# Performance work log

Hardware: AMD Instinct MI355X
Metric: run time of the kernel (lower is better)

Reference implementation:

```python
import jax, jax.numpy as jnp
import numpy as np

B, S, D, H = 2, 2048, 768, 12
DK = D // H

def setup_inputs() -> dict:
    key = jax.random.key(0)
    ks = jax.random.split(key, 8)
    query = jax.random.normal(ks[0], (B, S, D), dtype=jnp.float32)
    key_t = jax.random.normal(ks[1], (B, S, D), dtype=jnp.float32)
    value = jax.random.normal(ks[2], (B, S, D), dtype=jnp.float32)
    # causal (look-ahead) mask: True above the diagonal -> masked
    mask = jnp.triu(jnp.ones((S, S), dtype=bool), k=1)[None, None]  # (1,1,S,S)
    scale = 1.0 / np.sqrt(D)
    w_q = jax.random.normal(ks[3], (D, D), dtype=jnp.float32) * scale
    w_k = jax.random.normal(ks[4], (D, D), dtype=jnp.float32) * scale
    w_v = jax.random.normal(ks[5], (D, D), dtype=jnp.float32) * scale
    w_o = jax.random.normal(ks[6], (D, D), dtype=jnp.float32) * scale
    return {"query": query, "key": key_t, "value": value, "mask": mask,
            "w_q": w_q, "w_k": w_k, "w_v": w_v, "w_o": w_o}

def reference(query, key, value, mask, w_q, w_k, w_v, w_o):
    b = query.shape[0]
    # nn.Linear(bias=False): y = x @ W.T
    q = (query @ w_q.T).reshape(b, -1, H, DK).transpose(0, 2, 1, 3)  # (B,H,Sq,dk)
    k = (key @ w_k.T).reshape(b, -1, H, DK).transpose(0, 2, 1, 3)    # (B,H,Sk,dk)
    v = (value @ w_v.T).reshape(b, -1, H, DK).transpose(0, 2, 1, 3)  # (B,H,Sk,dk)
    scores = jnp.einsum('bhqd,bhkd->bhqk', q, k) / jnp.sqrt(jnp.float32(DK))
    scores = jnp.where(mask, jnp.float32(-1e9), scores)
    attn_weights = jax.nn.softmax(scores, axis=-1)  # (B,H,Sq,Sk); dropout=0 (eval)
    context = jnp.einsum('bhqk,bhkd->bhqd', attn_weights, v)
    context = context.transpose(0, 2, 1, 3).reshape(b, -1, D)
    output = context @ w_o.T
    return output, attn_weights
```

## Files before the change

### kernel.cpp

```cpp
#include <hip/hip_runtime.h>

#define BATCH 2
#define S_LEN 2048
#define NH 12
#define DMODEL 768

#define N8_BSD (BATCH * S_LEN * DMODEL / 8)
#define N8_DD (DMODEL * DMODEL / 8)

typedef __attribute__((ext_vector_type(8))) short bf16x8;
typedef __attribute__((ext_vector_type(4))) float f32x4;
typedef __attribute__((ext_vector_type(4))) unsigned short us4;

__device__ __forceinline__ unsigned short f2bf(float f) {
  union { float f; unsigned int u; } v; v.f = f;
  unsigned int r = v.u + 0x7fffu + ((v.u >> 16) & 1u);
  return (unsigned short)(r >> 16);
}

__global__ void cvt3_kernel(const float* __restrict__ s0,
                            const float* __restrict__ s1,
                            const float* __restrict__ s2,
                            unsigned short* __restrict__ dst) {
  int i = blockIdx.x * blockDim.x + threadIdx.x;
  int j = i / N8_BSD;
  int k = i - j * N8_BSD;
  const float* s = (j == 0) ? s0 : (j == 1) ? s1 : s2;
  const float4* sp = (const float4*)s;
  float4 a = sp[k * 2], b = sp[k * 2 + 1];
  us4 o0 = { f2bf(a.x), f2bf(a.y), f2bf(a.z), f2bf(a.w) };
  us4 o1 = { f2bf(b.x), f2bf(b.y), f2bf(b.z), f2bf(b.w) };
  us4* d = (us4*)dst;
  d[i * 2] = o0;
  d[i * 2 + 1] = o1;
}

__global__ void cvt4_kernel(const float* __restrict__ s0,
                            const float* __restrict__ s1,
                            const float* __restrict__ s2,
                            const float* __restrict__ s3,
                            unsigned short* __restrict__ dst) {
  int i = blockIdx.x * blockDim.x + threadIdx.x;
  int j = i / N8_DD;
  int k = i - j * N8_DD;
  const float* s = (j == 0) ? s0 : (j == 1) ? s1 : (j == 2) ? s2 : s3;
  const float4* sp = (const float4*)s;
  float4 a = sp[k * 2], b = sp[k * 2 + 1];
  us4 o0 = { f2bf(a.x), f2bf(a.y), f2bf(a.z), f2bf(a.w) };
  us4 o1 = { f2bf(b.x), f2bf(b.y), f2bf(b.z), f2bf(b.w) };
  us4* d = (us4*)dst;
  d[i * 2] = o0;
  d[i * 2 + 1] = o1;
}

__global__ void ctx_reduce(const float* __restrict__ c0,
                           const float* __restrict__ c1,
                           unsigned short* __restrict__ o) {
  int i = blockIdx.x * blockDim.x + threadIdx.x;
  int s = (i / 192) & (S_LEN - 1);
  float4 a = ((const float4*)c0)[i];
  float4 r = a;
  if (s >= 1024) {
    float4 b = ((const float4*)c1)[i];
    r.x += b.x; r.y += b.y; r.z += b.z; r.w += b.w;
  }
  us4 u = { f2bf(r.x), f2bf(r.y), f2bf(r.z), f2bf(r.w) };
  ((us4*)o)[i] = u;
}

#define GLD_LDS16(g, l)                                                    \
  __builtin_amdgcn_global_load_lds(                                        \
      (const __attribute__((address_space(1))) unsigned int*)(g),          \
      (__attribute__((address_space(3))) unsigned int*)(l), 16, 0, 0)

__global__ __launch_bounds__(256, 2)
void gemm_qkv(const unsigned short* __restrict__ Aq,
              const unsigned short* __restrict__ Ak,
              const unsigned short* __restrict__ Av,
              const unsigned short* __restrict__ W3,
              unsigned short* __restrict__ Qs,
              unsigned short* __restrict__ Ks,
              unsigned short* __restrict__ VT) {
  __shared__ unsigned short As[128 * 64];
  __shared__ unsigned short Bs[128 * 64];
  const int m0 = blockIdx.x * 128;
  const int n0g = blockIdx.y * 128;
  const int nblk = n0g / 768;
  const int n0 = n0g - nblk * 768;
  const unsigned short* A = (nblk == 0) ? Aq : (nblk == 1) ? Ak : Av;
  const unsigned short* Bw = W3 + (size_t)n0g * DMODEL;
  const int tid = threadIdx.x, w = tid >> 6, l = tid & 63;
  const int lg = l >> 4, ll = l & 15;
  const int wm = w >> 1, wn = w & 1;
  const int lr = l >> 3, lc = (l & 7) * 8;

  f32x4 acc[4][4];
#pragma unroll
  for (int i = 0; i < 4; ++i)
#pragma unroll
    for (int j = 0; j < 4; ++j) acc[i][j] = (f32x4){0.f, 0.f, 0.f, 0.f};

  for (int k0 = 0; k0 < DMODEL; k0 += 64) {
#pragma unroll
    for (int i = 0; i < 4; ++i) {
      GLD_LDS16(A + (size_t)(m0 + w * 32 + i * 8 + lr) * DMODEL + k0 + lc,
                &As[(w * 32 + i * 8) * 64]);
      GLD_LDS16(Bw + (size_t)(w * 32 + i * 8 + lr) * DMODEL + k0 + lc,
                &Bs[(w * 32 + i * 8) * 64]);
    }
    __syncthreads();
#pragma unroll
    for (int t = 0; t < 2; ++t) {
      bf16x8 af[4], bf[4];
#pragma unroll
      for (int mi = 0; mi < 4; ++mi)
        af[mi] = *(const bf16x8*)&As[(wm * 64 + mi * 16 + ll) * 64 + t * 32 + lg * 8];
#pragma unroll
      for (int ni = 0; ni < 4; ++ni)
        bf[ni] = *(const bf16x8*)&Bs[(wn * 64 + ni * 16 + ll) * 64 + t * 32 + lg * 8];
#pragma unroll
      for (int mi = 0; mi < 4; ++mi)
#pragma unroll
        for (int ni = 0; ni < 4; ++ni)
          acc[mi][ni] = __builtin_amdgcn_mfma_f32_16x16x32_bf16(
              af[mi], bf[ni], acc[mi][ni], 0, 0, 0);
    }
    __syncthreads();
  }

  if (nblk < 2) {
    unsigned short* o = nblk ? Ks : Qs;
    const float sc = nblk ? 1.f : 0.125f;
#pragma unroll
    for (int mi = 0; mi < 4; ++mi)
#pragma unroll
      for (int ni = 0; ni < 4; ++ni) {
        const int col = n0 + wn * 64 + ni * 16 + ll;
        const int rowb = m0 + wm * 64 + mi * 16 + lg * 4;
#pragma unroll
        for (int r = 0; r < 4; ++r)
          o[(size_t)(rowb + r) * 768 + col] = f2bf(acc[mi][ni][r] * sc);
      }
  } else {
#pragma unroll
    for (int mi = 0; mi < 4; ++mi)
#pragma unroll
      for (int ni = 0; ni < 4; ++ni) {
        const int col = n0 + wn * 64 + ni * 16 + ll;
        const int row = m0 + wm * 64 + mi * 16 + lg * 4;
        const int bb = row >> 11, sidx = row & (S_LEN - 1);
        const size_t base =
            ((size_t)(bb * NH + (col >> 6)) * 64 + (col & 63)) * S_LEN + sidx;
        us4 pk = { f2bf(acc[mi][ni][0]), f2bf(acc[mi][ni][1]),
                   f2bf(acc[mi][ni][2]), f2bf(acc[mi][ni][3]) };
        *(us4*)&VT[base] = pk;
      }
  }
}

__global__ __launch_bounds__(256, 2)
void gemm_proj(const unsigned short* __restrict__ A,
               const unsigned short* __restrict__ Bw,
               float* __restrict__ o) {
  __shared__ unsigned short As[128 * 64];
  __shared__ unsigned short Bs[128 * 64];
  const int m0 = blockIdx.x * 128, n0 = blockIdx.y * 128;
  const int tid = threadIdx.x, w = tid >> 6, l = tid & 63;
  const int lg = l >> 4, ll = l & 15;
  const int wm = w >> 1, wn = w & 1;
  const int lr = l >> 3, lc = (l & 7) * 8;

  f32x4 acc[4][4];
#pragma unroll
  for (int i = 0; i < 4; ++i)
#pragma unroll
    for (int j = 0; j < 4; ++j) acc[i][j] = (f32x4){0.f, 0.f, 0.f, 0.f};

  for (int k0 = 0; k0 < DMODEL; k0 += 64) {
#pragma unroll
    for (int i = 0; i < 4; ++i) {
      GLD_LDS16(A + (size_t)(m0 + w * 32 + i * 8 + lr) * DMODEL + k0 + lc,
                &As[(w * 32 + i * 8) * 64]);
      GLD_LDS16(Bw + (size_t)(n0 + w * 32 + i * 8 + lr) * DMODEL + k0 + lc,
                &Bs[(w * 32 + i * 8) * 64]);
    }
    __syncthreads();
#pragma unroll
    for (int t = 0; t < 2; ++t) {
      bf16x8 af[4], bf[4];
#pragma unroll
      for (int mi = 0; mi < 4; ++mi)
        af[mi] = *(const bf16x8*)&As[(wm * 64 + mi * 16 + ll) * 64 + t * 32 + lg * 8];
#pragma unroll
      for (int ni = 0; ni < 4; ++ni)
        bf[ni] = *(const bf16x8*)&Bs[(wn * 64 + ni * 16 + ll) * 64 + t * 32 + lg * 8];
#pragma unroll
      for (int mi = 0; mi < 4; ++mi)
#pragma unroll
        for (int ni = 0; ni < 4; ++ni)
          acc[mi][ni] = __builtin_amdgcn_mfma_f32_16x16x32_bf16(
              af[mi], bf[ni], acc[mi][ni], 0, 0, 0);
    }
    __syncthreads();
  }

#pragma unroll
  for (int mi = 0; mi < 4; ++mi)
#pragma unroll
    for (int ni = 0; ni < 4; ++ni) {
      const int col = n0 + wn * 64 + ni * 16 + ll;
      const int rowb = m0 + wm * 64 + mi * 16 + lg * 4;
#pragma unroll
      for (int r = 0; r < 4; ++r)
        o[(size_t)(rowb + r) * DMODEL + col] = acc[mi][ni][r];
    }
}

#define STAGE_TILE(srcTile, srcStride, ldsT)                                  \
  {                                                                           \
    _Pragma("unroll") for (int j_ = 0; j_ < 2; ++j_) {                        \
      int slot_ = (j_ * 4 + w) * 64 + l;                                      \
      int row_ = slot_ >> 3, c16_ = slot_ & 7;                                \
      GLD_LDS16((srcTile) + (size_t)row_ * (srcStride) +                      \
                    ((c16_ ^ (row_ & 7)) << 3),                               \
                (ldsT) + (j_ * 4 + w) * 512);                                 \
    }                                                                         \
  }

__global__ __launch_bounds__(256, 3)
void attn_ml(const unsigned short* __restrict__ Qp,
             const unsigned short* __restrict__ Kp,
             float2* __restrict__ mlbuf) {
  const int idx = blockIdx.x;
  const int qt = 31 - idx / (NH * BATCH);
  const int hb = idx % (NH * BATCH);
  const int h = hb >> 1, b = hb & 1;
  const int tid = threadIdx.x, w = tid >> 6, l = tid & 63;
  const int lg = l >> 4, ll = l & 15;
  __shared__ unsigned short Kt[2][64 * 64];

  const unsigned short* kbp = Kp + (size_t)b * S_LEN * DMODEL + h * 64;
  const int q0 = qt * 64 + w * 16;
  const int nkt = qt + 1;

  bf16x8 qf[2];
  {
    const unsigned short* qb =
        Qp + (size_t)(b * S_LEN + q0 + ll) * DMODEL + h * 64 + lg * 8;
    qf[0] = *(const bf16x8*)qb;
    qf[1] = *(const bf16x8*)(qb + 32);
  }
  int rowg[4];
#pragma unroll
  for (int r = 0; r < 4; ++r) rowg[r] = q0 + lg * 4 + r;

  float m[4], lsum[4];
#pragma unroll
  for (int r = 0; r < 4; ++r) { m[r] = -1e30f; lsum[r] = 0.f; }

  STAGE_TILE(kbp + (size_t)0 * 64 * DMODEL, DMODEL, &Kt[0][0]);
  __syncthreads();

  for (int kt = 0; kt < nkt; ++kt) {
    const int cur = kt & 1;
    if (kt + 1 < nkt)
      STAGE_TILE(kbp + (size_t)(kt + 1) * 64 * DMODEL, DMODEL, &Kt[cur ^ 1][0]);
    bf16x8 kf[8];
#pragma unroll
    for (int t = 0; t < 2; ++t)
#pragma unroll
      for (int nb = 0; nb < 4; ++nb) {
        const int row = nb * 16 + ll;
        kf[t * 4 + nb] = *(const bf16x8*)&Kt[cur][row * 64 +
            (((t * 4 + lg) ^ (row & 7)) << 3)];
      }
    f32x4 sv[4];
#pragma unroll
    for (int nb = 0; nb < 4; ++nb) sv[nb] = (f32x4){0.f, 0.f, 0.f, 0.f};
#pragma unroll
    for (int t = 0; t < 2; ++t)
#pragma unroll
      for (int nb = 0; nb < 4; ++nb)
        sv[nb] = __builtin_amdgcn_mfma_f32_16x16x32_bf16(qf[t], kf[t * 4 + nb],
                                                         sv[nb], 0, 0, 0);
    if (kt == nkt - 1) {
#pragma unroll
      for (int nb = 0; nb < 4; ++nb) {
        const int col = kt * 64 + nb * 16 + ll;
#pragma unroll
        for (int r = 0; r < 4; ++r)
          if (col > rowg[r]) sv[nb][r] = -1e30f;
      }
    }
#pragma unroll
    for (int r = 0; r < 4; ++r) {
      float tm = fmaxf(fmaxf(sv[0][r], sv[1][r]), fmaxf(sv[2][r], sv[3][r]));
      float mn = fmaxf(m[r], tm);
      float te = __expf(sv[0][r] - mn) + __expf(sv[1][r] - mn) +
                 __expf(sv[2][r] - mn) + __expf(sv[3][r] - mn);
      lsum[r] = lsum[r] * __expf(m[r] - mn) + te;
      m[r] = mn;
    }
    __syncthreads();
  }

#pragma unroll
  for (int off = 1; off < 16; off <<= 1)
#pragma unroll
    for (int r = 0; r < 4; ++r) {
      float om = __shfl_xor(m[r], off, 64);
      float ol = __shfl_xor(lsum[r], off, 64);
      float mn = fmaxf(m[r], om);
      lsum[r] = lsum[r] * __expf(m[r] - mn) + ol * __expf(om - mn);
      m[r] = mn;
    }

  if (ll == 0) {
    float2* mlb = mlbuf + (size_t)(b * NH + h) * S_LEN;
#pragma unroll
    for (int r = 0; r < 4; ++r)
      mlb[rowg[r]] = make_float2(m[r], 1.f / lsum[r]);
  }
}

__global__ __launch_bounds__(256, 2)
void attn_p2(const unsigned short* __restrict__ Qp,
             const unsigned short* __restrict__ Kp,
             const unsigned short* __restrict__ VTp,
             const float2* __restrict__ mlbuf,
             float* __restrict__ attnw,
             float* __restrict__ ctx0,
             float* __restrict__ ctx1) {
  const int idx = blockIdx.x;
  const int hb = idx >> 6;
  const int slot = idx & 63;
  const int h = hb >> 1, b = hb & 1;
  int qt, ck;
  if (slot <= 16)      { ck = 0; qt = 15 + slot; }
  else if (slot == 17) { ck = 1; qt = 31; }
  else if (slot < 48)  { int u = slot - 18; int k = 15 - (u >> 1);
                         if (u & 1) { ck = 1; qt = k + 15; } else { ck = 0; qt = k - 1; } }
  else                 { ck = 1; qt = slot - 48; }

  const int ktlo = ck * 16;
  const int kthi = (qt < ktlo + 15) ? qt : (ktlo + 15);
  const bool hasval = (ktlo <= qt);

  const int tid = threadIdx.x, w = tid >> 6, l = tid & 63;
  const int lg = l >> 4, ll = l & 15;
  __shared__ float pf32[4][64 * 64];
  float* pfw = &pf32[w][0];

  const unsigned short* kbp = Kp + (size_t)b * S_LEN * DMODEL + h * 64;
  const unsigned short* vbp = VTp + ((size_t)(b * NH + h)) * 64 * S_LEN;
  float* pbase = attnw + ((size_t)(b * NH + h)) * S_LEN * S_LEN;
  const int q0g = qt * 64;

  if (hasval) {
    bf16x8 qf[4][2];
#pragma unroll
    for (int rb = 0; rb < 4; ++rb) {
      const unsigned short* qb =
          Qp + (size_t)(b * S_LEN + q0g + rb * 16 + ll) * DMODEL + h * 64 + lg * 8;
      qf[rb][0] = *(const bf16x8*)qb;
      qf[rb][1] = *(const bf16x8*)(qb + 32);
    }
    float m16[4][4], li16[4][4];
    {
      const float2* mlb = mlbuf + (size_t)(b * NH + h) * S_LEN;
#pragma unroll
      for (int rb = 0; rb < 4; ++rb)
#pragma unroll
        for (int r = 0; r < 4; ++r) {
          float2 t = mlb[q0g + rb * 16 + lg * 4 + r];
          m16[rb][r] = t.x;
          li16[rb][r] = t.y;
        }
    }

    f32x4 cacc[4][4];
#pragma unroll
    for (int rb = 0; rb < 4; ++rb)
#pragma unroll
      for (int vb = 0; vb < 4; ++vb) cacc[rb][vb] = (f32x4){0.f, 0.f, 0.f, 0.f};

    for (int kt = ktlo + w; kt <= kthi; kt += 4) {
#pragma unroll
      for (int hh = 0; hh < 2; ++hh) {
        bf16x8 kf[2][2];
#pragma unroll
        for (int t = 0; t < 2; ++t)
#pragma unroll
          for (int nbl = 0; nbl < 2; ++nbl) {
            const int nb = hh * 2 + nbl;
            kf[t][nbl] = *(const bf16x8*)(kbp +
                (size_t)(kt * 64 + nb * 16 + ll) * DMODEL + t * 32 + lg * 8);
          }
        f32x4 sv[4][2];
#pragma unroll
        for (int rb = 0; rb < 4; ++rb)
#pragma unroll
          for (int nbl = 0; nbl < 2; ++nbl) sv[rb][nbl] = (f32x4){0.f, 0.f, 0.f, 0.f};
#pragma unroll
        for (int t = 0; t < 2; ++t)
#pragma unroll
          for (int rb = 0; rb < 4; ++rb)
#pragma unroll
            for (int nbl = 0; nbl < 2; ++nbl)
              sv[rb][nbl] = __builtin_amdgcn_mfma_f32_16x16x32_bf16(
                  qf[rb][t], kf[t][nbl], sv[rb][nbl], 0, 0, 0);
#pragma unroll
        for (int nbl = 0; nbl < 2; ++nbl) {
          const int nb = hh * 2 + nbl;
          const int col = kt * 64 + nb * 16 + ll;
#pragma unroll
          for (int rb = 0; rb < 4; ++rb)
#pragma unroll
            for (int r = 0; r < 4; ++r) {
              const int row = q0g + rb * 16 + lg * 4 + r;
              float p = (col <= row)
                            ? __expf(sv[rb][nbl][r] - m16[rb][r]) * li16[rb][r]
                            : 0.f;
              pfw[(rb * 16 + lg * 4 + r) * 64 +
                  ((nb * 16 + ll) ^ ((lg & 1) << 4))] = p;
            }
        }
      }
#pragma unroll
      for (int t = 0; t < 2; ++t) {
        bf16x8 pfr[4];
#pragma unroll
        for (int rb = 0; rb < 4; ++rb) {
          const int row = rb * 16 + ll;
          const int c0 = (t * 32 + lg * 8) ^ (((ll >> 2) & 1) << 4);
          f32x4 lo = *(const f32x4*)&pfw[row * 64 + c0];
          f32x4 hi = *(const f32x4*)&pfw[row * 64 + c0 + 4];
          union { us4 hh2[2]; bf16x8 v; } u;
          u.hh2[0] = (us4){ f2bf(lo[0]), f2bf(lo[1]), f2bf(lo[2]), f2bf(lo[3]) };
          u.hh2[1] = (us4){ f2bf(hi[0]), f2bf(hi[1]), f2bf(hi[2]), f2bf(hi[3]) };
          pfr[rb] = u.v;
        }
        bf16x8 vf[4];
#pragma unroll
        for (int vb = 0; vb < 4; ++vb)
          vf[vb] = *(const bf16x8*)(vbp +
              (size_t)(vb * 16 + ll) * S_LEN + kt * 64 + t * 32 + lg * 8);
#pragma unroll
        for (int rb = 0; rb < 4; ++rb)
#pragma unroll
          for (int vb = 0; vb < 4; ++vb)
            cacc[rb][vb] = __builtin_amdgcn_mfma_f32_16x16x32_bf16(
                pfr[rb], vf[vb], cacc[rb][vb], 0, 0, 0);
      }
#pragma unroll
      for (int ps = 0; ps < 16; ++ps) {
        const int row = ps * 4 + lg;
        const int cb = (ll * 4) ^ ((ps & 1) << 4);
        f32x4 pv = *(const f32x4*)&pfw[row * 64 + cb];
        __builtin_nontemporal_store(
            pv, (f32x4*)&pbase[(size_t)(q0g + row) * S_LEN + kt * 64 + ll * 4]);
      }
    }

#pragma unroll
    for (int rb = 0; rb < 4; ++rb)
#pragma unroll
      for (int vb = 0; vb < 4; ++vb)
#pragma unroll
        for (int r = 0; r < 4; ++r)
          pfw[(rb * 16 + lg * 4 + r) * 64 +
              ((vb * 16 + ll) ^ ((lg & 1) << 4))] = cacc[rb][vb][r];
    __syncthreads();
    float* co = ck ? ctx1 : ctx0;
#pragma unroll
    for (int ps2 = 0; ps2 < 4; ++ps2) {
      const int row = w * 16 + ps2 * 4 + lg;
      const int cb = (ll * 4) ^ ((ps2 & 1) << 4);
      f32x4 s0 = *(const f32x4*)&pf32[0][row * 64 + cb];
      f32x4 s1 = *(const f32x4*)&pf32[1][row * 64 + cb];
      f32x4 s2 = *(const f32x4*)&pf32[2][row * 64 + cb];
      f32x4 s3 = *(const f32x4*)&pf32[3][row * 64 + cb];
      f32x4 sm = (s0 + s1) + (s2 + s3);
      *(f32x4*)&co[(size_t)(b * S_LEN + q0g + row) * DMODEL + h * 64 + ll * 4] = sm;
    }
  }

  const int q0w = qt * 64 + w * 16;
  const int zs = ((qt + 1) * 64 > ktlo * 64) ? (qt + 1) * 64 : ktlo * 64;
  const int ze = (ktlo + 16) * 64;
  if (zs < ze) {
    f32x4 z = (f32x4){0.f, 0.f, 0.f, 0.f};
    for (int rr = 0; rr < 16; ++rr) {
      float* dst = pbase + (size_t)(q0w + rr) * S_LEN;
      for (int c = zs + l * 4; c < ze; c += 256)
        __builtin_nontemporal_store(z, (f32x4*)(dst + c));
    }
  }
}

extern "C" void kernel_launch(void* const* d_in, const int* in_sizes, int n_in,
                              void* d_out, int out_size, void* d_ws, size_t ws_size,
                              hipStream_t stream) {
  const float* q_in = (const float*)d_in[0];
  const float* k_in = (const float*)d_in[1];
  const float* v_in = (const float*)d_in[2];
  const float* wq = (const float*)d_in[4];
  const float* wk = (const float*)d_in[5];
  const float* wv = (const float*)d_in[6];
  const float* wo = (const float*)d_in[7];

  const int BSD = BATCH * S_LEN * DMODEL;
  const int DD = DMODEL * DMODEL;
  const int M = BATCH * S_LEN;

  char* ws = (char*)d_ws;
  unsigned short* qbf = (unsigned short*)ws;  ws += (size_t)BSD * 2;
  unsigned short* kbf = (unsigned short*)ws;  ws += (size_t)BSD * 2;
  unsigned short* vbf = (unsigned short*)ws;  ws += (size_t)BSD * 2;
  unsigned short* wqb = (unsigned short*)ws;  ws += (size_t)DD * 2;
  unsigned short* wkb = (unsigned short*)ws;  ws += (size_t)DD * 2;
  unsigned short* wvb = (unsigned short*)ws;  ws += (size_t)DD * 2;
  unsigned short* wob = (unsigned short*)ws;  ws += (size_t)DD * 2;
  unsigned short* Qs  = (unsigned short*)ws;  ws += (size_t)BSD * 2;
  unsigned short* Ks  = (unsigned short*)ws;  ws += (size_t)BSD * 2;
  unsigned short* VT  = (unsigned short*)ws;  ws += (size_t)BSD * 2;
  unsigned short* ctx = (unsigned short*)ws;  ws += (size_t)BSD * 2;
  float* ctx0 = (float*)ws;                   ws += (size_t)BSD * 4;
  float* ctx1 = (float*)ws;                   ws += (size_t)BSD * 4;
  float2* mlbuf = (float2*)ws;                ws += (size_t)M * NH * sizeof(float2);
  (void)wkb; (void)wvb;

  float* out_proj = (float*)d_out;
  float* attnw = (float*)d_out + BSD;

  cvt3_kernel<<<3 * N8_BSD / 256, 256, 0, stream>>>(q_in, k_in, v_in, qbf);
  cvt4_kernel<<<4 * N8_DD / 256, 256, 0, stream>>>(wq, wk, wv, wo, wqb);

  gemm_qkv<<<dim3(M / 128, 2304 / 128), 256, 0, stream>>>(qbf, kbf, vbf, wqb,
                                                          Qs, Ks, VT);

  attn_ml<<<32 * NH * BATCH, 256, 0, stream>>>(Qs, Ks, mlbuf);
  attn_p2<<<64 * NH * BATCH, 256, 0, stream>>>(Qs, Ks, VT, mlbuf, attnw,
                                               ctx0, ctx1);
  ctx_reduce<<<BSD / 4 / 256, 256, 0, stream>>>(ctx0, ctx1, ctx);

  gemm_proj<<<dim3(M / 128, DMODEL / 128), 256, 0, stream>>>(ctx, wob, out_proj);
}
```

Baseline: 189.7 us.

## Split attention p2 blocks into 32-row query halves and reorder ml grid

The attn_p2 kernel now processes 32 query rows per block instead of 64. This doubles the grid, halves shared memory per block and cuts register pressure, so launch bounds can request 3 blocks per CU. Each K tile is still loaded once per 32-row block, so K/V global loads per output row double, traded for better occupancy and load balance. The attn_ml block index mapping is also changed so that consecutive blocks share a head and batch, which is meant to improve K locality in cache.

```diff
diff --git a/kernel.cpp b/kernel.cpp
--- a/kernel.cpp
+++ b/kernel.cpp
@@ -232,8 +232,8 @@
              const unsigned short* __restrict__ Kp,
              float2* __restrict__ mlbuf) {
   const int idx = blockIdx.x;
-  const int qt = 31 - idx / (NH * BATCH);
-  const int hb = idx % (NH * BATCH);
+  const int hb = idx >> 5;
+  const int qt = 31 - (idx & 31);
   const int h = hb >> 1, b = hb & 1;
   const int tid = threadIdx.x, w = tid >> 6, l = tid & 63;
   const int lg = l >> 4, ll = l & 15;
@@ -323,7 +323,7 @@
   }
 }
 
-__global__ __launch_bounds__(256, 2)
+__global__ __launch_bounds__(256, 3)
 void attn_p2(const unsigned short* __restrict__ Qp,
              const unsigned short* __restrict__ Kp,
              const unsigned short* __restrict__ VTp,
@@ -332,8 +332,10 @@
              float* __restrict__ ctx0,
              float* __restrict__ ctx1) {
   const int idx = blockIdx.x;
-  const int hb = idx >> 6;
-  const int slot = idx & 63;
+  const int hb = idx >> 7;
+  const int sl = idx & 127;
+  const int slot = sl >> 1;
+  const int qh = sl & 1;
   const int h = hb >> 1, b = hb & 1;
   int qt, ck;
   if (slot <= 16)      { ck = 0; qt = 15 + slot; }
@@ -348,28 +350,28 @@
 
   const int tid = threadIdx.x, w = tid >> 6, l = tid & 63;
   const int lg = l >> 4, ll = l & 15;
-  __shared__ float pf32[4][64 * 64];
+  __shared__ float pf32[4][32 * 64];
   float* pfw = &pf32[w][0];
 
   const unsigned short* kbp = Kp + (size_t)b * S_LEN * DMODEL + h * 64;
   const unsigned short* vbp = VTp + ((size_t)(b * NH + h)) * 64 * S_LEN;
   float* pbase = attnw + ((size_t)(b * NH + h)) * S_LEN * S_LEN;
-  const int q0g = qt * 64;
+  const int q0g = qt * 64 + qh * 32;
 
   if (hasval) {
-    bf16x8 qf[4][2];
-#pragma unroll
-    for (int rb = 0; rb < 4; ++rb) {
+    bf16x8 qf[2][2];
+#pragma unroll
+    for (int rb = 0; rb < 2; ++rb) {
       const unsigned short* qb =
           Qp + (size_t)(b * S_LEN + q0g + rb * 16 + ll) * DMODEL + h * 64 + lg * 8;
       qf[rb][0] = *(const bf16x8*)qb;
       qf[rb][1] = *(const bf16x8*)(qb + 32);
     }
-    float m16[4][4], li16[4][4];
+    float m16[2][4], li16[2][4];
     {
       const float2* mlb = mlbuf + (size_t)(b * NH + h) * S_LEN;
 #pragma unroll
-      for (int rb = 0; rb < 4; ++rb)
+      for (int rb = 0; rb < 2; ++rb)
 #pragma unroll
         for (int r = 0; r < 4; ++r) {
           float2 t = mlb[q0g + rb * 16 + lg * 4 + r];
@@ -378,59 +380,53 @@
         }
     }
 
-    f32x4 cacc[4][4];
-#pragma unroll
-    for (int rb = 0; rb < 4; ++rb)
+    f32x4 cacc[2][4];
+#pragma unroll
+    for (int rb = 0; rb < 2; ++rb)
 #pragma unroll
       for (int vb = 0; vb < 4; ++vb) cacc[rb][vb] = (f32x4){0.f, 0.f, 0.f, 0.f};
 
     for (int kt = ktlo + w; kt <= kthi; kt += 4) {
-#pragma unroll
-      for (int hh = 0; hh < 2; ++hh) {
-        bf16x8 kf[2][2];
-#pragma unroll
-        for (int t = 0; t < 2; ++t)
-#pragma unroll
-          for (int nbl = 0; nbl < 2; ++nbl) {
-            const int nb = hh * 2 + nbl;
-            kf[t][nbl] = *(const bf16x8*)(kbp +
-                (size_t)(kt * 64 + nb * 16 + ll) * DMODEL + t * 32 + lg * 8);
+      bf16x8 kf[2][4];
+#pragma unroll
+      for (int t = 0; t < 2; ++t)
+#pragma unroll
+        for (int nb = 0; nb < 4; ++nb)
+          kf[t][nb] = *(const bf16x8*)(kbp +
+              (size_t)(kt * 64 + nb * 16 + ll) * DMODEL + t * 32 + lg * 8);
+      f32x4 sv[2][4];
+#pragma unroll
+      for (int rb = 0; rb < 2; ++rb)
+#pragma unroll
+        for (int nb = 0; nb < 4; ++nb) sv[rb][nb] = (f32x4){0.f, 0.f, 0.f, 0.f};
+#pragma unroll
+      for (int t = 0; t < 2; ++t)
+#pragma unroll
+        for (int rb = 0; rb < 2; ++rb)
+#pragma unroll
+          for (int nb = 0; nb < 4; ++nb)
+            sv[rb][nb] = __builtin_amdgcn_mfma_f32_16x16x32_bf16(
+                qf[rb][t], kf[t][nb], sv[rb][nb], 0, 0, 0);
+#pragma unroll
+      for (int nb = 0; nb < 4; ++nb) {
+        const int col = kt * 64 + nb * 16 + ll;
+#pragma unroll
+        for (int rb = 0; rb < 2; ++rb)
+#pragma unroll
+          for (int r = 0; r < 4; ++r) {
+            const int row = q0g + rb * 16 + lg * 4 + r;
+            float p = (col <= row)
+                          ? __expf(sv[rb][nb][r] - m16[rb][r]) * li16[rb][r]
+                          : 0.f;
+            pfw[(rb * 16 + lg * 4 + r) * 64 +
+                ((nb * 16 + ll) ^ ((lg & 1) << 4))] = p;
           }
-        f32x4 sv[4][2];
-#pragma unroll
-        for (int rb = 0; rb < 4; ++rb)
-#pragma unroll
-          for (int nbl = 0; nbl < 2; ++nbl) sv[rb][nbl] = (f32x4){0.f, 0.f, 0.f, 0.f};
-#pragma unroll
-        for (int t = 0; t < 2; ++t)
-#pragma unroll
-          for (int rb = 0; rb < 4; ++rb)
-#pragma unroll
-            for (int nbl = 0; nbl < 2; ++nbl)
-              sv[rb][nbl] = __builtin_amdgcn_mfma_f32_16x16x32_bf16(
-                  qf[rb][t], kf[t][nbl], sv[rb][nbl], 0, 0, 0);
-#pragma unroll
-        for (int nbl = 0; nbl < 2; ++nbl) {
-          const int nb = hh * 2 + nbl;
-          const int col = kt * 64 + nb * 16 + ll;
-#pragma unroll
-          for (int rb = 0; rb < 4; ++rb)
-#pragma unroll
-            for (int r = 0; r < 4; ++r) {
-              const int row = q0g + rb * 16 + lg * 4 + r;
-              float p = (col <= row)
-                            ? __expf(sv[rb][nbl][r] - m16[rb][r]) * li16[rb][r]
-                            : 0.f;
-              pfw[(rb * 16 + lg * 4 + r) * 64 +
-                  ((nb * 16 + ll) ^ ((lg & 1) << 4))] = p;
-            }
-        }
       }
 #pragma unroll
       for (int t = 0; t < 2; ++t) {
-        bf16x8 pfr[4];
-#pragma unroll
-        for (int rb = 0; rb < 4; ++rb) {
+        bf16x8 pfr[2];
+#pragma unroll
+        for (int rb = 0; rb < 2; ++rb) {
           const int row = rb * 16 + ll;
           const int c0 = (t * 32 + lg * 8) ^ (((ll >> 2) & 1) << 4);
           f32x4 lo = *(const f32x4*)&pfw[row * 64 + c0];
@@ -446,24 +442,24 @@
           vf[vb] = *(const bf16x8*)(vbp +
               (size_t)(vb * 16 + ll) * S_LEN + kt * 64 + t * 32 + lg * 8);
 #pragma unroll
-        for (int rb = 0; rb < 4; ++rb)
+        for (int rb = 0; rb < 2; ++rb)
 #pragma unroll
           for (int vb = 0; vb < 4; ++vb)
             cacc[rb][vb] = __builtin_amdgcn_mfma_f32_16x16x32_bf16(
                 pfr[rb], vf[vb], cacc[rb][vb], 0, 0, 0);
       }
 #pragma unroll
-      for (int ps = 0; ps < 16; ++ps) {
-        const int row = ps * 4 + lg;
+      for (int ps = 0; ps < 8; ++ps) {
+        const int lrow = ps * 4 + lg;
         const int cb = (ll * 4) ^ ((ps & 1) << 4);
-        f32x4 pv = *(const f32x4*)&pfw[row * 64 + cb];
+        f32x4 pv = *(const f32x4*)&pfw[lrow * 64 + cb];
         __builtin_nontemporal_store(
-            pv, (f32x4*)&pbase[(size_t)(q0g + row) * S_LEN + kt * 64 + ll * 4]);
-      }
-    }
-
-#pragma unroll
-    for (int rb = 0; rb < 4; ++rb)
+            pv, (f32x4*)&pbase[(size_t)(q0g + lrow) * S_LEN + kt * 64 + ll * 4]);
+      }
+    }
+
+#pragma unroll
+    for (int rb = 0; rb < 2; ++rb)
 #pragma unroll
       for (int vb = 0; vb < 4; ++vb)
 #pragma unroll
@@ -473,25 +469,24 @@
     __syncthreads();
     float* co = ck ? ctx1 : ctx0;
 #pragma unroll
-    for (int ps2 = 0; ps2 < 4; ++ps2) {
-      const int row = w * 16 + ps2 * 4 + lg;
+    for (int ps2 = 0; ps2 < 2; ++ps2) {
+      const int lrow = w * 8 + ps2 * 4 + lg;
       const int cb = (ll * 4) ^ ((ps2 & 1) << 4);
-      f32x4 s0 = *(const f32x4*)&pf32[0][row * 64 + cb];
-      f32x4 s1 = *(const f32x4*)&pf32[1][row * 64 + cb];
-      f32x4 s2 = *(const f32x4*)&pf32[2][row * 64 + cb];
-      f32x4 s3 = *(const f32x4*)&pf32[3][row * 64 + cb];
+      f32x4 s0 = *(const f32x4*)&pf32[0][lrow * 64 + cb];
+      f32x4 s1 = *(const f32x4*)&pf32[1][lrow * 64 + cb];
+      f32x4 s2 = *(const f32x4*)&pf32[2][lrow * 64 + cb];
+      f32x4 s3 = *(const f32x4*)&pf32[3][lrow * 64 + cb];
       f32x4 sm = (s0 + s1) + (s2 + s3);
-      *(f32x4*)&co[(size_t)(b * S_LEN + q0g + row) * DMODEL + h * 64 + ll * 4] = sm;
-    }
-  }
-
-  const int q0w = qt * 64 + w * 16;
+      *(f32x4*)&co[(size_t)(b * S_LEN + q0g + lrow) * DMODEL + h * 64 + ll * 4] = sm;
+    }
+  }
+
   const int zs = ((qt + 1) * 64 > ktlo * 64) ? (qt + 1) * 64 : ktlo * 64;
   const int ze = (ktlo + 16) * 64;
   if (zs < ze) {
     f32x4 z = (f32x4){0.f, 0.f, 0.f, 0.f};
-    for (int rr = 0; rr < 16; ++rr) {
-      float* dst = pbase + (size_t)(q0w + rr) * S_LEN;
+    for (int rr = 0; rr < 8; ++rr) {
+      float* dst = pbase + (size_t)(q0g + w * 8 + rr) * S_LEN;
       for (int c = zs + l * 4; c < ze; c += 256)
         __builtin_nontemporal_store(z, (f32x4*)(dst + c));
     }
@@ -540,8 +535,8 @@
                                                           Qs, Ks, VT);
 
   attn_ml<<<32 * NH * BATCH, 256, 0, stream>>>(Qs, Ks, mlbuf);
-  attn_p2<<<64 * NH * BATCH, 256, 0, stream>>>(Qs, Ks, VT, mlbuf, attnw,
-                                               ctx0, ctx1);
+  attn_p2<<<128 * NH * BATCH, 256, 0, stream>>>(Qs, Ks, VT, mlbuf, attnw,
+                                                ctx0, ctx1);
   ctx_reduce<<<BSD / 4 / 256, 256, 0, stream>>>(ctx0, ctx1, ctx);
 
   gemm_proj<<<dim3(M / 128, DMODEL / 128), 256, 0, stream>>>(ctx, wob, out_proj);
```

After: 187.2 us. No clear change (-1.4%).
